# Performance work log

Hardware: AMD Instinct MI355X
Metric: run time of the kernel (lower is better)

The kernel has to match this reference:

```python
import jax, jax.numpy as jnp
import numpy as np

NUM_HEADS = 8
NG = 8  # group/grid size: seq = NG**3 = 512


def setup_inputs() -> dict:
    key = jax.random.key(0)
    k1, k2, k3 = jax.random.split(key, 3)
    batch, seq, chan = 32, NG ** 3, 512
    subspace_dim = 24
    x = jax.random.normal(k1, (batch, seq, chan), jnp.float32)
    # fixed symmetric-subspace basis (the free variable `conv_kernel` in the source)
    basis = jax.random.normal(k2, (seq, subspace_dim), jnp.float32)
    # learned param: (subspace_dim, num_heads), init stddev 0.01
    kernel = jax.random.normal(k3, (subspace_dim, NUM_HEADS), jnp.float32) * 0.01
    return {"x": x, "basis": basis, "kernel": kernel}


def reference(x, basis, kernel):
    batch, seq, chan = x.shape
    h, ng = NUM_HEADS, NG
    kn = 2 * ng - 1  # 15: circular tiling window
    ch = chan // h
    # 'batch (8 8 8) (ch h) -> h (batch ch) 8 8 8'
    x_im = x.reshape(batch, ng, ng, ng, ch, h)
    x_im = jnp.transpose(x_im, (5, 0, 4, 1, 2, 3)).reshape(h, batch * ch, ng, ng, ng)
    # circular tiling: tile 2x2x2 then crop to 2*ng-1 per axis; add trailing C=1
    x_im = jnp.tile(x_im, (1, 1, 2, 2, 2))[:, :, :kn, :kn, :kn, None]
    # expand subspace kernel: '(n n n) s, s h -> h n n n 1 1'
    kexp = jnp.einsum('gs,sh->hg', basis, kernel).reshape(h, ng, ng, ng, 1, 1)

    def conv(lhs, rhs):
        return jax.lax.conv_general_dilated(
            lhs, rhs, window_strides=(1, 1, 1), padding='VALID',
            dimension_numbers=('NXYZC', 'XYZIO', 'NXYZC'))

    # per-head VALID conv: [batch*ch, 15,15,15, 1] * [8,8,8,1,1] -> [batch*ch, 8,8,8, 1]
    out = jax.vmap(conv)(x_im, kexp)[..., 0]  # [h, batch*ch, 8, 8, 8]
    # 'h (batch ch) n n n -> batch (n n n) (ch h)'
    out = out.reshape(h, batch, ch, seq)
    out = jnp.transpose(out, (1, 3, 2, 0)).reshape(batch, seq, chan)
    return out
```

## Files before the change

kernel.cpp:

```cpp
#include <hip/hip_runtime.h>


#define S2C 0.70710678118654752f
#define ST2 20
#define ST1 164
#define STP 1312

template <bool INV>
__device__ __forceinline__ void dft8(float* R, float* I)
{
    float t0r = R[0] + R[4], t0i = I[0] + I[4];
    float t1r = R[1] + R[5], t1i = I[1] + I[5];
    float t2r = R[2] + R[6], t2i = I[2] + I[6];
    float t3r = R[3] + R[7], t3i = I[3] + I[7];
    float b0r = R[0] - R[4], b0i = I[0] - I[4];
    float d1r = R[1] - R[5], d1i = I[1] - I[5];
    float d2r = R[2] - R[6], d2i = I[2] - I[6];
    float d3r = R[3] - R[7], d3i = I[3] - I[7];
    float b1r, b1i, b2r, b2i, b3r, b3i;
    if (!INV) {
        b1r = (d1r + d1i) * S2C;  b1i = (d1i - d1r) * S2C;
        b2r = d2i;                b2i = -d2r;
        b3r = (d3i - d3r) * S2C;  b3i = -(d3r + d3i) * S2C;
    } else {
        b1r = (d1r - d1i) * S2C;  b1i = (d1i + d1r) * S2C;
        b2r = -d2i;               b2i = d2r;
        b3r = -(d3r + d3i) * S2C; b3i = (d3r - d3i) * S2C;
    }
    float u0r = t0r + t2r, u0i = t0i + t2i;
    float u1r = t1r + t3r, u1i = t1i + t3i;
    float u2r = t0r - t2r, u2i = t0i - t2i;
    float e3r = t1r - t3r, e3i = t1i - t3i;
    float u3r, u3i;
    if (!INV) { u3r = e3i;  u3i = -e3r; }
    else      { u3r = -e3i; u3i = e3r;  }
    R[0] = u0r + u1r; I[0] = u0i + u1i;
    R[4] = u0r - u1r; I[4] = u0i - u1i;
    R[2] = u2r + u3r; I[2] = u2i + u3i;
    R[6] = u2r - u3r; I[6] = u2i - u3i;
    float v0r = b0r + b2r, v0i = b0i + b2i;
    float v1r = b1r + b3r, v1i = b1i + b3i;
    float v2r = b0r - b2r, v2i = b0i - b2i;
    float w3r = b1r - b3r, w3i = b1i - b3i;
    float v3r, v3i;
    if (!INV) { v3r = w3i;  v3i = -w3r; }
    else      { v3r = -w3i; v3i = w3r;  }
    R[1] = v0r + v1r; I[1] = v0i + v1i;
    R[5] = v0r - v1r; I[5] = v0i - v1i;
    R[3] = v2r + v3r; I[3] = v2i + v3i;
    R[7] = v2r - v3r; I[7] = v2i - v3i;
}

__device__ const float CTAB8[8] = {1.f, S2C, 0.f, -S2C, -1.f, -S2C, 0.f, S2C};
__device__ const float STAB8[8] = {0.f, S2C, 1.f, S2C, 0.f, -S2C, -1.f, -S2C};

__global__ __launch_bounds__(256)
void eqfft_prep(const float* __restrict__ basis,
                const float* __restrict__ kparam,
                float2* __restrict__ V)
{
    __shared__ float Wl[512];
    __shared__ float CT[8], ST[8];
    const int tid = threadIdx.x;
    const int blk = blockIdx.x;
    const int h   = blk >> 4;
    if (tid < 8) { CT[tid] = CTAB8[tid]; ST[tid] = STAB8[tid]; }
    #pragma unroll
    for (int t = 0; t < 2; ++t) {
        const int g = tid * 2 + t;
        const float* bp = basis + g * 24;
        float acc = 0.f;
        #pragma unroll
        for (int s = 0; s < 24; ++s) acc += bp[s] * kparam[s * 8 + h];
        Wl[(g & 63) * 8 + (g >> 6)] = acc;
    }
    __syncthreads();
    const int f  = (blk & 15) * 32 + (tid >> 3);
    const int g1 = tid & 7;
    const int f1 = f >> 6, f2 = (f >> 3) & 7, f3 = f & 7;
    const int kb = (f1 * g1) & 7;
    float pr = 0.f, pi = 0.f;
    for (int g2 = 0; g2 < 8; ++g2) {
        const int k2 = kb + f2 * g2;
        const float* wrow = &Wl[g2 * 64 + g1];
        #pragma unroll
        for (int g3 = 0; g3 < 8; ++g3) {
            const int k = (k2 + f3 * g3) & 7;
            const float w = wrow[g3 * 8];
            pr += w * CT[k];
            pi += w * ST[k];
        }
    }
    pr += __shfl_xor(pr, 1); pi += __shfl_xor(pi, 1);
    pr += __shfl_xor(pr, 2); pi += __shfl_xor(pi, 2);
    pr += __shfl_xor(pr, 4); pi += __shfl_xor(pi, 4);
    if (g1 == 0)
        V[h * 512 + f] = make_float2(pr * (1.f / 512.f), pi * (1.f / 512.f));
}

__global__ __launch_bounds__(256, 3)
void eqfft_main(const float* __restrict__ x,
                const float2* __restrict__ V,
                float* __restrict__ out)
{
    __shared__ __align__(16) float reA[4 * STP];
    __shared__ __align__(16) float imA[4 * STP];

    const int tid = threadIdx.x;
    const int bid = blockIdx.x;
    const int b   = bid >> 6;
    const int ch0 = (bid & 63) * 8;

    const float* xb = x   + (size_t)b * 262144 + ch0;
    float*       ob = out + (size_t)b * 262144 + ch0;

    #pragma unroll
    for (int i = 0; i < 4; ++i) {
        const int v  = i * 256 + tid;
        const int pt = v >> 1;
        const int c4 = (v & 1) * 4;
        const float4 d = *(const float4*)(xb + pt * 512 + c4);
        const int base = (pt >> 6) * ST1 + ((pt >> 3) & 7) * ST2 + (pt & 7) * 2;
        const int pr = c4 >> 1;
        *(float2*)(reA + pr * STP + base)       = make_float2(d.x, d.y);
        *(float2*)(reA + (pr + 1) * STP + base) = make_float2(d.z, d.w);
    }
    __syncthreads();

    const int pair = tid >> 6;
    const int line = tid & 63;
    float R0[8], I0[8], R1[8], I1[8];

    {
        float* rp = reA + pair * STP + (line >> 3) * ST1 + (line & 7) * ST2;
        float* ip = imA + pair * STP + (line >> 3) * ST1 + (line & 7) * ST2;
        #pragma unroll
        for (int k = 0; k < 4; ++k) {
            const float4 d = *(const float4*)(rp + 4 * k);
            R0[2*k] = d.x; R1[2*k] = d.y; R0[2*k+1] = d.z; R1[2*k+1] = d.w;
            I0[2*k] = 0.f; I1[2*k] = 0.f; I0[2*k+1] = 0.f; I1[2*k+1] = 0.f;
        }
        dft8<false>(R0, I0); dft8<false>(R1, I1);
        #pragma unroll
        for (int k = 0; k < 4; ++k) {
            *(float4*)(rp + 4*k) = make_float4(R0[2*k], R1[2*k], R0[2*k+1], R1[2*k+1]);
            *(float4*)(ip + 4*k) = make_float4(I0[2*k], I1[2*k], I0[2*k+1], I1[2*k+1]);
        }
    }
    __syncthreads();

    {
        float* rp = reA + pair * STP + (line >> 3) * ST1 + (line & 7) * 2;
        float* ip = imA + pair * STP + (line >> 3) * ST1 + (line & 7) * 2;
        #pragma unroll
        for (int j = 0; j < 8; ++j) {
            const float2 a = *(const float2*)(rp + j * ST2);
            const float2 c = *(const float2*)(ip + j * ST2);
            R0[j] = a.x; R1[j] = a.y; I0[j] = c.x; I1[j] = c.y;
        }
        dft8<false>(R0, I0); dft8<false>(R1, I1);
        #pragma unroll
        for (int j = 0; j < 8; ++j) {
            *(float2*)(rp + j * ST2) = make_float2(R0[j], R1[j]);
            *(float2*)(ip + j * ST2) = make_float2(I0[j], I1[j]);
        }
    }
    __syncthreads();

    {
        const int p2 = line >> 3, p3 = line & 7;
        const float2* v0 = V + (pair * 2 + 0) * 512 + p2 * 8 + p3;
        const float2* v1 = V + (pair * 2 + 1) * 512 + p2 * 8 + p3;
        float2 va[8], vb[8];
        #pragma unroll
        for (int j = 0; j < 8; ++j) { va[j] = v0[j << 6]; vb[j] = v1[j << 6]; }

        float* rp = reA + pair * STP + p2 * ST2 + p3 * 2;
        float* ip = imA + pair * STP + p2 * ST2 + p3 * 2;
        #pragma unroll
        for (int j = 0; j < 8; ++j) {
            const float2 a = *(const float2*)(rp + j * ST1);
            const float2 c = *(const float2*)(ip + j * ST1);
            R0[j] = a.x; R1[j] = a.y; I0[j] = c.x; I1[j] = c.y;
        }
        dft8<false>(R0, I0); dft8<false>(R1, I1);
        #pragma unroll
        for (int j = 0; j < 8; ++j) {
            float nr = R0[j] * va[j].x - I0[j] * va[j].y;
            I0[j]    = R0[j] * va[j].y + I0[j] * va[j].x;
            R0[j]    = nr;
            nr       = R1[j] * vb[j].x - I1[j] * vb[j].y;
            I1[j]    = R1[j] * vb[j].y + I1[j] * vb[j].x;
            R1[j]    = nr;
        }
        dft8<true>(R0, I0); dft8<true>(R1, I1);
        #pragma unroll
        for (int j = 0; j < 8; ++j) {
            *(float2*)(rp + j * ST1) = make_float2(R0[j], R1[j]);
            *(float2*)(ip + j * ST1) = make_float2(I0[j], I1[j]);
        }
    }
    __syncthreads();

    {
        float* rp = reA + pair * STP + (line >> 3) * ST1 + (line & 7) * 2;
        float* ip = imA + pair * STP + (line >> 3) * ST1 + (line & 7) * 2;
        #pragma unroll
        for (int j = 0; j < 8; ++j) {
            const float2 a = *(const float2*)(rp + j * ST2);
            const float2 c = *(const float2*)(ip + j * ST2);
            R0[j] = a.x; R1[j] = a.y; I0[j] = c.x; I1[j] = c.y;
        }
        dft8<true>(R0, I0); dft8<true>(R1, I1);
        #pragma unroll
        for (int j = 0; j < 8; ++j) {
            *(float2*)(rp + j * ST2) = make_float2(R0[j], R1[j]);
            *(float2*)(ip + j * ST2) = make_float2(I0[j], I1[j]);
        }
    }
    __syncthreads();

    {
        float* rp = reA + pair * STP + (line >> 3) * ST1 + (line & 7) * ST2;
        float* ip = imA + pair * STP + (line >> 3) * ST1 + (line & 7) * ST2;
        #pragma unroll
        for (int k = 0; k < 4; ++k) {
            const float4 a = *(const float4*)(rp + 4 * k);
            const float4 c = *(const float4*)(ip + 4 * k);
            R0[2*k] = a.x; R1[2*k] = a.y; R0[2*k+1] = a.z; R1[2*k+1] = a.w;
            I0[2*k] = c.x; I1[2*k] = c.y; I0[2*k+1] = c.z; I1[2*k+1] = c.w;
        }
        dft8<true>(R0, I0); dft8<true>(R1, I1);
        #pragma unroll
        for (int k = 0; k < 4; ++k)
            *(float4*)(rp + 4*k) = make_float4(R0[2*k], R1[2*k], R0[2*k+1], R1[2*k+1]);
    }
    __syncthreads();

    #pragma unroll
    for (int i = 0; i < 4; ++i) {
        const int v  = i * 256 + tid;
        const int pt = v >> 1;
        const int c4 = (v & 1) * 4;
        const int base = (pt >> 6) * ST1 + ((pt >> 3) & 7) * ST2 + (pt & 7) * 2;
        const int pr = c4 >> 1;
        const float2 a = *(const float2*)(reA + pr * STP + base);
        const float2 c = *(const float2*)(reA + (pr + 1) * STP + base);
        *(float4*)(ob + pt * 512 + c4) = make_float4(a.x, a.y, c.x, c.y);
    }
}

extern "C" void kernel_launch(void* const* d_in, const int* in_sizes, int n_in,
                              void* d_out, int out_size, void* d_ws, size_t ws_size,
                              hipStream_t stream)
{
    const float* x      = (const float*)d_in[0];
    const float* basis  = (const float*)d_in[1];
    const float* kparam = (const float*)d_in[2];
    float* out          = (float*)d_out;
    float2* V           = (float2*)d_ws;

    hipLaunchKernelGGL(eqfft_prep, dim3(128),  dim3(256), 0, stream, basis, kparam, V);
    hipLaunchKernelGGL(eqfft_main, dim3(2048), dim3(256), 0, stream, x, V, out);
}
```

Baseline: 113.8 us.

## Pack two same-head real channels into one complex FFT per lane

Each block now covers 16 channels instead of 8. Channels c and c+8 share a head, so they are loaded as the real and imaginary parts of one complex 3D signal. The convolution kernel is real, so one complex FFT, pointwise multiply and inverse FFT give both channels' circular convolutions at once, roughly halving FFT arithmetic and LDS traffic per channel. The LDS layout becomes interleaved complex with new padding strides, and launch bounds rise to 4 blocks per CU; register pressure and bank conflicts from the new strides are the risk.

```diff
diff --git a/kernel.cpp b/kernel.cpp
--- a/kernel.cpp
+++ b/kernel.cpp
@@ -2,9 +2,9 @@
 
 
 #define S2C 0.70710678118654752f
-#define ST2 20
-#define ST1 164
-#define STP 1312
+#define S2  18
+#define S1  146
+#define CST 1172
 
 template <bool INV>
 __device__ __forceinline__ void dft8(float* R, float* I)
@@ -98,90 +98,96 @@
         V[h * 512 + f] = make_float2(pr * (1.f / 512.f), pi * (1.f / 512.f));
 }
 
-__global__ __launch_bounds__(256, 3)
+__global__ __launch_bounds__(256, 4)
 void eqfft_main(const float* __restrict__ x,
                 const float2* __restrict__ V,
                 float* __restrict__ out)
 {
-    __shared__ __align__(16) float reA[4 * STP];
-    __shared__ __align__(16) float imA[4 * STP];
+    __shared__ __align__(16) float lds[8 * CST];
 
     const int tid = threadIdx.x;
     const int bid = blockIdx.x;
-    const int b   = bid >> 6;
-    const int ch0 = (bid & 63) * 8;
-
-    const float* xb = x   + (size_t)b * 262144 + ch0;
-    float*       ob = out + (size_t)b * 262144 + ch0;
+    const int b   = bid >> 5;
+    const int c0  = (bid & 31) * 16;
+
+    const float* xb = x   + (size_t)b * 262144 + c0;
+    float*       ob = out + (size_t)b * 262144 + c0;
 
     #pragma unroll
-    for (int i = 0; i < 4; ++i) {
-        const int v  = i * 256 + tid;
-        const int pt = v >> 1;
-        const int c4 = (v & 1) * 4;
-        const float4 d = *(const float4*)(xb + pt * 512 + c4);
-        const int base = (pt >> 6) * ST1 + ((pt >> 3) & 7) * ST2 + (pt & 7) * 2;
-        const int pr = c4 >> 1;
-        *(float2*)(reA + pr * STP + base)       = make_float2(d.x, d.y);
-        *(float2*)(reA + (pr + 1) * STP + base) = make_float2(d.z, d.w);
-    }
-    __syncthreads();
-
-    const int pair = tid >> 6;
-    const int line = tid & 63;
+    for (int t = 0; t < 4; ++t) {
+        const int G = t * 256 + tid;
+        const int p = G >> 1;
+        const int u = G & 1;
+        const float4 A  = *(const float4*)(xb + p * 512 + u * 4);
+        const float4 Bv = *(const float4*)(xb + p * 512 + u * 4 + 8);
+        const int base = (p >> 6) * S1 + ((p >> 3) & 7) * S2 + (p & 7) * 2;
+        float* dst = lds + (u * 4) * CST + base;
+        *(float2*)(dst + 0 * CST) = make_float2(A.x, Bv.x);
+        *(float2*)(dst + 1 * CST) = make_float2(A.y, Bv.y);
+        *(float2*)(dst + 2 * CST) = make_float2(A.z, Bv.z);
+        *(float2*)(dst + 3 * CST) = make_float2(A.w, Bv.w);
+    }
+    __syncthreads();
+
+    const int q = tid >> 5;
+    const int e = tid & 31;
     float R0[8], I0[8], R1[8], I1[8];
 
     {
-        float* rp = reA + pair * STP + (line >> 3) * ST1 + (line & 7) * ST2;
-        float* ip = imA + pair * STP + (line >> 3) * ST1 + (line & 7) * ST2;
-        #pragma unroll
-        for (int k = 0; k < 4; ++k) {
-            const float4 d = *(const float4*)(rp + 4 * k);
-            R0[2*k] = d.x; R1[2*k] = d.y; R0[2*k+1] = d.z; R1[2*k+1] = d.w;
-            I0[2*k] = 0.f; I1[2*k] = 0.f; I0[2*k+1] = 0.f; I1[2*k+1] = 0.f;
+        const int P0 = 2 * e, P1 = 2 * e + 1;
+        float* pa = lds + q * CST + (P0 >> 3) * S1 + (P0 & 7) * S2;
+        float* pb = lds + q * CST + (P1 >> 3) * S1 + (P1 & 7) * S2;
+        #pragma unroll
+        for (int j = 0; j < 8; ++j) {
+            const float2 za = *(const float2*)(pa + 2 * j);
+            const float2 zb = *(const float2*)(pb + 2 * j);
+            R0[j] = za.x; I0[j] = za.y; R1[j] = zb.x; I1[j] = zb.y;
         }
         dft8<false>(R0, I0); dft8<false>(R1, I1);
         #pragma unroll
-        for (int k = 0; k < 4; ++k) {
-            *(float4*)(rp + 4*k) = make_float4(R0[2*k], R1[2*k], R0[2*k+1], R1[2*k+1]);
-            *(float4*)(ip + 4*k) = make_float4(I0[2*k], I1[2*k], I0[2*k+1], I1[2*k+1]);
-        }
-    }
-    __syncthreads();
-
-    {
-        float* rp = reA + pair * STP + (line >> 3) * ST1 + (line & 7) * 2;
-        float* ip = imA + pair * STP + (line >> 3) * ST1 + (line & 7) * 2;
-        #pragma unroll
-        for (int j = 0; j < 8; ++j) {
-            const float2 a = *(const float2*)(rp + j * ST2);
-            const float2 c = *(const float2*)(ip + j * ST2);
-            R0[j] = a.x; R1[j] = a.y; I0[j] = c.x; I1[j] = c.y;
+        for (int j = 0; j < 8; ++j) {
+            *(float2*)(pa + 2 * j) = make_float2(R0[j], I0[j]);
+            *(float2*)(pb + 2 * j) = make_float2(R1[j], I1[j]);
+        }
+    }
+    __syncthreads();
+
+    {
+        const int P0 = 2 * e, P1 = 2 * e + 1;
+        float* pa = lds + q * CST + (P0 >> 3) * S1 + (P0 & 7) * 2;
+        float* pb = lds + q * CST + (P1 >> 3) * S1 + (P1 & 7) * 2;
+        #pragma unroll
+        for (int j = 0; j < 8; ++j) {
+            const float2 za = *(const float2*)(pa + S2 * j);
+            const float2 zb = *(const float2*)(pb + S2 * j);
+            R0[j] = za.x; I0[j] = za.y; R1[j] = zb.x; I1[j] = zb.y;
         }
         dft8<false>(R0, I0); dft8<false>(R1, I1);
         #pragma unroll
         for (int j = 0; j < 8; ++j) {
-            *(float2*)(rp + j * ST2) = make_float2(R0[j], R1[j]);
-            *(float2*)(ip + j * ST2) = make_float2(I0[j], I1[j]);
-        }
-    }
-    __syncthreads();
-
-    {
-        const int p2 = line >> 3, p3 = line & 7;
-        const float2* v0 = V + (pair * 2 + 0) * 512 + p2 * 8 + p3;
-        const float2* v1 = V + (pair * 2 + 1) * 512 + p2 * 8 + p3;
+            *(float2*)(pa + S2 * j) = make_float2(R0[j], I0[j]);
+            *(float2*)(pb + S2 * j) = make_float2(R1[j], I1[j]);
+        }
+    }
+    __syncthreads();
+
+    {
+        const int P0 = 2 * e, P1 = 2 * e + 1;
+        const int p2a = P0 >> 3, p3a = P0 & 7;
+        const int p2b = P1 >> 3, p3b = P1 & 7;
+        const float2* v0 = V + q * 512 + p2a * 8 + p3a;
+        const float2* v1 = V + q * 512 + p2b * 8 + p3b;
         float2 va[8], vb[8];
         #pragma unroll
         for (int j = 0; j < 8; ++j) { va[j] = v0[j << 6]; vb[j] = v1[j << 6]; }
 
-        float* rp = reA + pair * STP + p2 * ST2 + p3 * 2;
-        float* ip = imA + pair * STP + p2 * ST2 + p3 * 2;
-        #pragma unroll
-        for (int j = 0; j < 8; ++j) {
-            const float2 a = *(const float2*)(rp + j * ST1);
-            const float2 c = *(const float2*)(ip + j * ST1);
-            R0[j] = a.x; R1[j] = a.y; I0[j] = c.x; I1[j] = c.y;
+        float* pa = lds + q * CST + p2a * S2 + p3a * 2;
+        float* pb = lds + q * CST + p2b * S2 + p3b * 2;
+        #pragma unroll
+        for (int j = 0; j < 8; ++j) {
+            const float2 za = *(const float2*)(pa + S1 * j);
+            const float2 zb = *(const float2*)(pb + S1 * j);
+            R0[j] = za.x; I0[j] = za.y; R1[j] = zb.x; I1[j] = zb.y;
         }
         dft8<false>(R0, I0); dft8<false>(R1, I1);
         #pragma unroll
@@ -196,57 +202,63 @@
         dft8<true>(R0, I0); dft8<true>(R1, I1);
         #pragma unroll
         for (int j = 0; j < 8; ++j) {
-            *(float2*)(rp + j * ST1) = make_float2(R0[j], R1[j]);
-            *(float2*)(ip + j * ST1) = make_float2(I0[j], I1[j]);
-        }
-    }
-    __syncthreads();
-
-    {
-        float* rp = reA + pair * STP + (line >> 3) * ST1 + (line & 7) * 2;
-        float* ip = imA + pair * STP + (line >> 3) * ST1 + (line & 7) * 2;
-        #pragma unroll
-        for (int j = 0; j < 8; ++j) {
-            const float2 a = *(const float2*)(rp + j * ST2);
-            const float2 c = *(const float2*)(ip + j * ST2);
-            R0[j] = a.x; R1[j] = a.y; I0[j] = c.x; I1[j] = c.y;
+            *(float2*)(pa + S1 * j) = make_float2(R0[j], I0[j]);
+            *(float2*)(pb + S1 * j) = make_float2(R1[j], I1[j]);
+        }
+    }
+    __syncthreads();
+
+    {
+        const int P0 = 2 * e, P1 = 2 * e + 1;
+        float* pa = lds + q * CST + (P0 >> 3) * S1 + (P0 & 7) * 2;
+        float* pb = lds + q * CST + (P1 >> 3) * S1 + (P1 & 7) * 2;
+        #pragma unroll
+        for (int j = 0; j < 8; ++j) {
+            const float2 za = *(const float2*)(pa + S2 * j);
+            const float2 zb = *(const float2*)(pb + S2 * j);
+            R0[j] = za.x; I0[j] = za.y; R1[j] = zb.x; I1[j] = zb.y;
         }
         dft8<true>(R0, I0); dft8<true>(R1, I1);
         #pragma unroll
         for (int j = 0; j < 8; ++j) {
-            *(float2*)(rp + j * ST2) = make_float2(R0[j], R1[j]);
-            *(float2*)(ip + j * ST2) = make_float2(I0[j], I1[j]);
-        }
-    }
-    __syncthreads();
-
-    {
-        float* rp = reA + pair * STP + (line >> 3) * ST1 + (line & 7) * ST2;
-        float* ip = imA + pair * STP + (line >> 3) * ST1 + (line & 7) * ST2;
-        #pragma unroll
-        for (int k = 0; k < 4; ++k) {
-            const float4 a = *(const float4*)(rp + 4 * k);
-            const float4 c = *(const float4*)(ip + 4 * k);
-            R0[2*k] = a.x; R1[2*k] = a.y; R0[2*k+1] = a.z; R1[2*k+1] = a.w;
-            I0[2*k] = c.x; I1[2*k] = c.y; I0[2*k+1] = c.z; I1[2*k+1] = c.w;
+            *(float2*)(pa + S2 * j) = make_float2(R0[j], I0[j]);
+            *(float2*)(pb + S2 * j) = make_float2(R1[j], I1[j]);
+        }
+    }
+    __syncthreads();
+
+    {
+        const int P0 = 2 * e, P1 = 2 * e + 1;
+        float* pa = lds + q * CST + (P0 >> 3) * S1 + (P0 & 7) * S2;
+        float* pb = lds + q * CST + (P1 >> 3) * S1 + (P1 & 7) * S2;
+        #pragma unroll
+        for (int j = 0; j < 8; ++j) {
+            const float2 za = *(const float2*)(pa + 2 * j);
+            const float2 zb = *(const float2*)(pb + 2 * j);
+            R0[j] = za.x; I0[j] = za.y; R1[j] = zb.x; I1[j] = zb.y;
         }
         dft8<true>(R0, I0); dft8<true>(R1, I1);
         #pragma unroll
-        for (int k = 0; k < 4; ++k)
-            *(float4*)(rp + 4*k) = make_float4(R0[2*k], R1[2*k], R0[2*k+1], R1[2*k+1]);
+        for (int j = 0; j < 8; ++j) {
+            *(float2*)(pa + 2 * j) = make_float2(R0[j], I0[j]);
+            *(float2*)(pb + 2 * j) = make_float2(R1[j], I1[j]);
+        }
     }
     __syncthreads();
 
     #pragma unroll
-    for (int i = 0; i < 4; ++i) {
-        const int v  = i * 256 + tid;
-        const int pt = v >> 1;
-        const int c4 = (v & 1) * 4;
-        const int base = (pt >> 6) * ST1 + ((pt >> 3) & 7) * ST2 + (pt & 7) * 2;
-        const int pr = c4 >> 1;
-        const float2 a = *(const float2*)(reA + pr * STP + base);
-        const float2 c = *(const float2*)(reA + (pr + 1) * STP + base);
-        *(float4*)(ob + pt * 512 + c4) = make_float4(a.x, a.y, c.x, c.y);
+    for (int t = 0; t < 4; ++t) {
+        const int G = t * 256 + tid;
+        const int p = G >> 1;
+        const int u = G & 1;
+        const int base = (p >> 6) * S1 + ((p >> 3) & 7) * S2 + (p & 7) * 2;
+        const float* src = lds + (u * 4) * CST + base;
+        const float2 z0 = *(const float2*)(src + 0 * CST);
+        const float2 z1 = *(const float2*)(src + 1 * CST);
+        const float2 z2 = *(const float2*)(src + 2 * CST);
+        const float2 z3 = *(const float2*)(src + 3 * CST);
+        *(float4*)(ob + p * 512 + u * 4)     = make_float4(z0.x, z1.x, z2.x, z3.x);
+        *(float4*)(ob + p * 512 + u * 4 + 8) = make_float4(z0.y, z1.y, z2.y, z3.y);
     }
 }
 
@@ -261,5 +273,5 @@
     float2* V           = (float2*)d_ws;
 
     hipLaunchKernelGGL(eqfft_prep, dim3(128),  dim3(256), 0, stream, basis, kparam, V);
-    hipLaunchKernelGGL(eqfft_main, dim3(2048), dim3(256), 0, stream, x, V, out);
-}
+    hipLaunchKernelGGL(eqfft_main, dim3(1024), dim3(256), 0, stream, x, V, out);
+}
```

Result: faster. 99.74 us (-12.4%).
